# Kernel optimization log

Measured on AMD Instinct MI355X. Metric: run time of the kernel, lower is better.

The kernel has to match this reference:

```python
import jax, jax.numpy as jnp
import numpy as np

B, N, D, H, L, K, V = 2, 2048, 512, 8, 4, 32, 256
HD = D // H
MOD = 4294967296.0
SCALE = 1.0 / np.sqrt(HD)


def _ln(x, g, b):
    m = x.mean(-1, keepdims=True)
    v = ((x - m) ** 2).mean(-1, keepdims=True)
    return (x - m) * jax.lax.rsqrt(v + 1e-5) * g + b


def _expmap0(v, c):
    sc = jnp.sqrt(c)
    vn = jnp.maximum(jnp.linalg.norm(v, axis=-1, keepdims=True), 1e-8)
    return jnp.tanh(sc * vn) * v / (sc * vn)


def _knn_poincare(pos, c):
    xx = jnp.sum(pos ** 2, -1)                                    # [N]
    d2 = jnp.maximum(xx[:, None] + xx[None, :] - 2.0 * pos @ pos.T, 0.0)
    denom = (1.0 - c * xx)[:, None] * (1.0 - c * xx)[None, :] + 1e-8
    arg = jnp.maximum(1.0 + 2.0 * c * d2 / denom, 1.0)
    dist = jnp.arccosh(arg) / jnp.sqrt(c)                         # [N,N]
    neg_d, idx = jax.lax.top_k(-dist, K)                          # smallest-k
    return -neg_d, idx                                            # [N,K],[N,K]


def _forward(hashes, indices, emb, hash_proj, Wb, bb, log_c, pos_tangent,
             Wq, bq, Wk, bk, Wv, bv, Wo, bo, W1, b1, W2, b2,
             g1, be1, g2, be2, log_tau, Wout, bout):
    c = jnp.exp(log_c)
    char = emb[indices]                                           # [B,N,D]
    he = (hashes[..., None].astype(jnp.float32) / MOD) @ hash_proj  # [B,N,D]
    x = jnp.concatenate([char, he], -1) @ Wb + bb                 # [B,N,D]

    # kNN structure computed under no_grad in the original
    pos = _expmap0(jax.lax.stop_gradient(pos_tangent), jax.lax.stop_gradient(c))
    attn_dists, idx = _knn_poincare(pos, jax.lax.stop_gradient(c))  # shared over batch

    for i in range(L):
        xn = _ln(x, g1[i], be1[i])
        q = (xn @ Wq[i] + bq[i]).reshape(B, N, H, HD).transpose(0, 2, 1, 3)
        k = (xn @ Wk[i] + bk[i]).reshape(B, N, H, HD).transpose(0, 2, 1, 3)
        v = (xn @ Wv[i] + bv[i]).reshape(B, N, H, HD).transpose(0, 2, 1, 3)
        kg = k[:, :, idx, :]                                      # [B,H,N,K,HD]
        vg = v[:, :, idx, :]
        fs = jnp.einsum('bhnd,bhnkd->bhnk', q, kg) * SCALE
        gs = -attn_dists[None, None] / (jnp.exp(log_tau[i]) + 1e-8)
        p = jax.nn.softmax(fs + gs, axis=-1)                      # [B,H,N,K]
        ao = jnp.einsum('bhnk,bhnkd->bhnd', p, vg)
        ao = ao.transpose(0, 2, 1, 3).reshape(B, N, D)
        x = x + ao @ Wo[i] + bo[i]
        xn2 = _ln(x, g2[i], be2[i])
        x = x + jax.nn.gelu(xn2 @ W1[i] + b1[i], approximate=False) @ W2[i] + b2[i]

    return x[:, -1, :] @ Wout + bout                              # [B,V]


def setup_inputs():
    key = jax.random.key(0)
    ks = jax.random.split(key, 20)
    rn = lambda k, s, sc=0.02: jax.random.normal(k, s, jnp.float32) * sc
    z = lambda s: jnp.zeros(s, jnp.float32)
    o = lambda s: jnp.ones(s, jnp.float32)
    return {
        'hashes': jax.random.randint(ks[0], (B, N), 0, 1000000),
        'indices': jax.random.randint(ks[1], (B, N), 0, V),
        'emb': rn(ks[2], (V, D)),
        'hash_proj': rn(ks[3], (1, D)),
        'Wb': rn(ks[4], (2 * D, D)),
        'bb': z((D,)),
        'log_c': jnp.array(0.0, jnp.float32),
        'pos_tangent': rn(ks[5], (N, D)),
        'Wq': rn(ks[6], (L, D, D)), 'bq': z((L, D)),
        'Wk': rn(ks[7], (L, D, D)), 'bk': z((L, D)),
        'Wv': rn(ks[8], (L, D, D)), 'bv': z((L, D)),
        'Wo': rn(ks[9], (L, D, D)), 'bo': z((L, D)),
        'W1': rn(ks[10], (L, D, 4 * D)), 'b1': z((L, 4 * D)),
        'W2': rn(ks[11], (L, 4 * D, D)), 'b2': z((L, D)),
        'g1': o((L, D)), 'be1': z((L, D)),
        'g2': o((L, D)), 'be2': z((L, D)),
        'log_tau': z((L,)),
        'Wout': rn(ks[12], (D, V)), 'bout': z((V,)),
    }


def reference(hashes, indices, emb, hash_proj, Wb, bb, log_c, pos_tangent,
              Wq, bq, Wk, bk, Wv, bv, Wo, bo, W1, b1, W2, b2,
              g1, be1, g2, be2, log_tau, Wout, bout):
    return _forward(hashes, indices, emb, hash_proj, Wb, bb, log_c, pos_tangent,
                    Wq, bq, Wk, bk, Wv, bv, Wo, bo, W1, b1, W2, b2,
                    g1, be1, g2, be2, log_tau, Wout, bout)
```

## Files before the change

### kernel.cpp

```cpp
#include <hip/hip_runtime.h>
#include <hip/hip_bf16.h>
#include <math.h>

#define Bb 2
#define Nn 2048
#define Dd 512
#define Hh 8
#define Ll 4
#define Kk 32
#define Vv 256
#define HDh 64
#define Mrows (Bb*Nn)

static constexpr float SCALE_QK = 0.125f;
static constexpr float INV_MOD = 1.0f / 4294967296.0f;

typedef _Float16 f16;
typedef _Float16 f16x8 __attribute__((ext_vector_type(8)));
typedef _Float16 f16x4 __attribute__((ext_vector_type(4)));
typedef _Float16 f16x2 __attribute__((ext_vector_type(2)));
typedef float f32x4 __attribute__((ext_vector_type(4)));

__global__ void scal_kernel(const float* __restrict__ log_c,
                            const float* __restrict__ log_tau,
                            float* __restrict__ scal) {
    int t = threadIdx.x;
    if (t == 0) {
        float c = expf(log_c[0]);
        scal[0] = c;
        scal[1] = sqrtf(c);
    }
    if (t < Ll) scal[2 + t] = 1.0f / (expf(log_tau[t]) + 1e-8f);
}

__global__ __launch_bounds__(256)
void hvec_part_kernel(const float* __restrict__ hash_proj,
                      const float* __restrict__ Wb,
                      float* __restrict__ part) {
    const int b = blockIdx.x;
    const int t = threadIdx.x;
    float a0 = 0.f, a1 = 0.f;
#pragma unroll
    for (int i = 0; i < 16; i++) {
        int kx = b * 16 + i;
        float hp = hash_proj[kx];
        const float* wr = Wb + (size_t)(Dd + kx) * Dd;
        a0 = fmaf(hp, wr[t], a0);
        a1 = fmaf(hp, wr[t + 256], a1);
    }
    part[b * Dd + t]       = a0;
    part[b * Dd + t + 256] = a1;
}
__global__ __launch_bounds__(256)
void hvec_red_kernel(const float* __restrict__ part, float* __restrict__ hvec) {
    const int n = blockIdx.x * 256 + threadIdx.x;
    float acc = 0.f;
#pragma unroll
    for (int b = 0; b < 32; b++) acc += part[b * Dd + n];
    hvec[n] = acc;
}

__global__ void conv_kernel(const float* __restrict__ src, f16* __restrict__ dst, int n) {
    int i = blockIdx.x * 256 + threadIdx.x;
    if (i < n) dst[i] = (f16)src[i];
}

__global__ void pack_bias_kernel(const float* __restrict__ bq, const float* __restrict__ bk,
                                 const float* __restrict__ bv, float* __restrict__ bqkv) {
    int t = blockIdx.x * 256 + threadIdx.x;
    int l = t / 1536, r = t % 1536;
    const float* src = (r < 512) ? bq : ((r < 1024) ? bk : bv);
    bqkv[t] = src[l * 512 + (r & 511)];
}

__global__ __launch_bounds__(256)
void trans_kernel(const float* __restrict__ src, f16* __restrict__ dst,
                  int K, int N, long sStride, long dStride) {
    __shared__ float tile[32][33];
    const float* s = src + blockIdx.z * sStride;
    f16* d = dst + blockIdx.z * dStride;
    int k0 = blockIdx.y * 32, n0 = blockIdx.x * 32;
    int tx = threadIdx.x & 31, ty = threadIdx.x >> 5;
#pragma unroll
    for (int i = 0; i < 32; i += 8)
        tile[ty + i][tx] = s[(long)(k0 + ty + i) * N + n0 + tx];
    __syncthreads();
#pragma unroll
    for (int i = 0; i < 32; i += 8)
        d[(long)(n0 + ty + i) * K + k0 + tx] = (f16)tile[tx][ty + i];
}

__global__ __launch_bounds__(256)
void trans4_kernel(const float* __restrict__ Wq, const float* __restrict__ Wk,
                   const float* __restrict__ Wv, const float* __restrict__ Wo,
                   f16* __restrict__ Wqkvt, f16* __restrict__ Wot) {
    __shared__ float tile[32][33];
    const int which = blockIdx.z >> 2, l = blockIdx.z & 3;
    const float* s;
    f16* d;
    switch (which) {
        case 0: s = Wq + (size_t)l * 262144; d = Wqkvt + (size_t)l * 786432;          break;
        case 1: s = Wk + (size_t)l * 262144; d = Wqkvt + (size_t)l * 786432 + 262144; break;
        case 2: s = Wv + (size_t)l * 262144; d = Wqkvt + (size_t)l * 786432 + 524288; break;
        default:s = Wo + (size_t)l * 262144; d = Wot   + (size_t)l * 262144;          break;
    }
    int k0 = blockIdx.y * 32, n0 = blockIdx.x * 32;
    int tx = threadIdx.x & 31, ty = threadIdx.x >> 5;
#pragma unroll
    for (int i = 0; i < 32; i += 8)
        tile[ty + i][tx] = s[(long)(k0 + ty + i) * 512 + n0 + tx];
    __syncthreads();
#pragma unroll
    for (int i = 0; i < 32; i += 8)
        d[(long)(n0 + ty + i) * 512 + k0 + tx] = (f16)tile[tx][ty + i];
}

template<int TN, bool GATHER, bool RANK1, bool GELU, bool RES, bool OUT16>
__global__ __launch_bounds__(256)
void mgemm(const f16* __restrict__ A, const f16* __restrict__ Wt,
           const float* __restrict__ bias,
           const int* __restrict__ gidx,
           const int* __restrict__ hashes, const float* __restrict__ hvec,
           const float* __restrict__ resid,
           void* __restrict__ Cout, int M, int N, int K) {
    constexpr int TM  = 64;
    constexpr int WRN = (TN == 64) ? 2 : 1;
    constexpr int WCN = 4 / WRN;
    constexpr int WRE = TM / WRN;
    constexpr int NIT = WRE / 16;
    constexpr int ACH = TM * 8;
    constexpr int BCH = TN * 8;
    constexpr int NCH = ACH + BCH;
    constexpr int NCHT = NCH / 256;
    __shared__ __align__(16) f16 sm[NCH * 8];
    const int t = threadIdx.x;
    const int lane = t & 63;
    const int w = t >> 6;
    const int wr = w / WCN, wc = w % WCN;
    const int i0 = blockIdx.y * TM, j0 = blockIdx.x * TN;

    const f16* gsrc[NCHT];
#pragma unroll
    for (int q = 0; q < NCHT; q++) {
        int c = t + q * 256;
        if (c < ACH) {
            int m = c >> 3, kb = (c & 7) ^ (m & 7);
            long row = GATHER ? (long)gidx[i0 + m] : (long)(i0 + m);
            gsrc[q] = A + row * K + kb * 8;
        } else {
            int cc = c - ACH;
            int n = cc >> 3, kb = (cc & 7) ^ (n & 7);
            gsrc[q] = Wt + (long)(j0 + n) * K + kb * 8;
        }
    }

    f32x4 acc[NIT][2];
#pragma unroll
    for (int i = 0; i < NIT; i++)
#pragma unroll
        for (int j = 0; j < 2; j++) acc[i][j] = (f32x4){0.f, 0.f, 0.f, 0.f};

    for (int kt = 0; kt < K; kt += 64) {
        f16x8 stg[NCHT];
#pragma unroll
        for (int q = 0; q < NCHT; q++) stg[q] = *(const f16x8*)(gsrc[q] + kt);
        __syncthreads();
#pragma unroll
        for (int q = 0; q < NCHT; q++)
            *(f16x8*)(sm + (t + q * 256) * 8) = stg[q];
        __syncthreads();

#pragma unroll
        for (int kh = 0; kh < 2; kh++) {
            f16x8 af[NIT], bf[2];
#pragma unroll
            for (int i = 0; i < NIT; i++) {
                int m = wr * WRE + i * 16 + (lane & 15);
                int sl = m * 8 + ((kh * 4 + (lane >> 4)) ^ (m & 7));
                af[i] = *(const f16x8*)(sm + sl * 8);
            }
#pragma unroll
            for (int j = 0; j < 2; j++) {
                int n = wc * 32 + j * 16 + (lane & 15);
                int sl = ACH + n * 8 + ((kh * 4 + (lane >> 4)) ^ (n & 7));
                bf[j] = *(const f16x8*)(sm + sl * 8);
            }
#pragma unroll
            for (int i = 0; i < NIT; i++)
#pragma unroll
                for (int j = 0; j < 2; j++)
                    acc[i][j] = __builtin_amdgcn_mfma_f32_16x16x32_f16(af[i], bf[j], acc[i][j], 0, 0, 0);
        }
    }

    float* Cf = (float*)Cout;
    f16*   Ch = (f16*)Cout;
#pragma unroll
    for (int i = 0; i < NIT; i++) {
        int rbase = i0 + wr * WRE + i * 16 + ((lane >> 4) << 2);
#pragma unroll
        for (int v = 0; v < 4; v++) {
            int row = rbase + v;
            float hterm = RANK1 ? (float)hashes[row] * INV_MOD : 0.f;
#pragma unroll
            for (int j = 0; j < 2; j++) {
                int col = j0 + wc * 32 + j * 16 + (lane & 15);
                float val = acc[i][j][v] + bias[col];
                if (RANK1) val += hterm * hvec[col];
                if (GELU)  val = 0.5f * val * (1.f + erff(val * 0.7071067811865475f));
                if (RES)   val += resid[(long)row * N + col];
                if (OUT16) Ch[(long)row * N + col] = (f16)val;
                else       Cf[(long)row * N + col] = val;
            }
        }
    }
}

__global__ __launch_bounds__(256)
void mdist_kernel(const f16* __restrict__ poshl, const float* __restrict__ xx,
                  const float* __restrict__ scal, float* __restrict__ dist) {
    constexpr int TM = 64, TN = 64;
    constexpr int ACH = TM * 8, BCH = TN * 8, NCH = ACH + BCH;
    constexpr int NCHT = NCH / 256;
    constexpr int KK = 1024;
    __shared__ __align__(16) f16 sm[NCH * 8];
    const int t = threadIdx.x;
    const int lane = t & 63;
    const int w = t >> 6;
    const int wr = w >> 1, wc = w & 1;
    const int i0 = blockIdx.y * TM, j0 = blockIdx.x * TN;

    const f16* gsrc[NCHT];
#pragma unroll
    for (int q = 0; q < NCHT; q++) {
        int c = t + q * 256;
        if (c < ACH) {
            int m = c >> 3, kb = (c & 7) ^ (m & 7);
            gsrc[q] = poshl + (long)(i0 + m) * KK + kb * 8;
        } else {
            int cc = c - ACH;
            int n = cc >> 3, kb = (cc & 7) ^ (n & 7);
            gsrc[q] = poshl + (long)(j0 + n) * KK + kb * 8;
        }
    }

    f32x4 acc[2][2];
#pragma unroll
    for (int i = 0; i < 2; i++)
#pragma unroll
        for (int j = 0; j < 2; j++) acc[i][j] = (f32x4){0.f, 0.f, 0.f, 0.f};

    for (int kt = 0; kt < KK; kt += 64) {
        f16x8 stg[NCHT];
#pragma unroll
        for (int q = 0; q < NCHT; q++) stg[q] = *(const f16x8*)(gsrc[q] + kt);
        __syncthreads();
#pragma unroll
        for (int q = 0; q < NCHT; q++)
            *(f16x8*)(sm + (t + q * 256) * 8) = stg[q];
        __syncthreads();

#pragma unroll
        for (int kh = 0; kh < 2; kh++) {
            f16x8 af[2], bf[2];
#pragma unroll
            for (int i = 0; i < 2; i++) {
                int m = wr * 32 + i * 16 + (lane & 15);
                int sl = m * 8 + ((kh * 4 + (lane >> 4)) ^ (m & 7));
                af[i] = *(const f16x8*)(sm + sl * 8);
            }
#pragma unroll
            for (int j = 0; j < 2; j++) {
                int n = wc * 32 + j * 16 + (lane & 15);
                int sl = ACH + n * 8 + ((kh * 4 + (lane >> 4)) ^ (n & 7));
                bf[j] = *(const f16x8*)(sm + sl * 8);
            }
#pragma unroll
            for (int i = 0; i < 2; i++)
#pragma unroll
                for (int j = 0; j < 2; j++)
                    acc[i][j] = __builtin_amdgcn_mfma_f32_16x16x32_f16(af[i], bf[j], acc[i][j], 0, 0, 0);
        }
    }

    const float c = scal[0];
#pragma unroll
    for (int i = 0; i < 2; i++) {
        int rbase = i0 + wr * 32 + i * 16 + ((lane >> 4) << 2);
#pragma unroll
        for (int v = 0; v < 4; v++) {
            int row = rbase + v;
            float xi = xx[row];
#pragma unroll
            for (int j = 0; j < 2; j++) {
                int col = j0 + wc * 32 + j * 16 + (lane & 15);
                float xj = xx[col];
                float d2 = fmaxf(xi + xj - 2.f * acc[i][j][v], 0.f);
                float denom = (1.f - c * xi) * (1.f - c * xj) + 1e-8f;
                float arg = fmaxf(1.f + 2.f * c * d2 / denom, 1.f);
                dist[(long)row * Nn + col] = arg;
            }
        }
    }
}

__global__ __launch_bounds__(64)
void ln_kernel(const float* __restrict__ x, const float* __restrict__ g,
               const float* __restrict__ be, f16* __restrict__ xn) {
    const int row = blockIdx.x, t = threadIdx.x;
    const float4* xr = (const float4*)(x + (size_t)row * Dd);
    float4 v0 = xr[t], v1 = xr[t + 64];
    float s = v0.x + v0.y + v0.z + v0.w + v1.x + v1.y + v1.z + v1.w;
#pragma unroll
    for (int off = 32; off; off >>= 1) s += __shfl_xor(s, off, 64);
    float mean = s * (1.f / Dd);
    float d0x = v0.x - mean, d0y = v0.y - mean, d0z = v0.z - mean, d0w = v0.w - mean;
    float d1x = v1.x - mean, d1y = v1.y - mean, d1z = v1.z - mean, d1w = v1.w - mean;
    float q = d0x*d0x + d0y*d0y + d0z*d0z + d0w*d0w
            + d1x*d1x + d1y*d1y + d1z*d1z + d1w*d1w;
#pragma unroll
    for (int off = 32; off; off >>= 1) q += __shfl_xor(q, off, 64);
    float rstd = rsqrtf(q * (1.f / Dd) + 1e-5f);
    float4 g0 = ((const float4*)g)[t], g1v = ((const float4*)g)[t + 64];
    float4 b0 = ((const float4*)be)[t], b1v = ((const float4*)be)[t + 64];
    f16* xo = xn + (size_t)row * Dd;
    f16x4 o0, o1;
    o0[0] = (f16)(d0x * rstd * g0.x + b0.x);
    o0[1] = (f16)(d0y * rstd * g0.y + b0.y);
    o0[2] = (f16)(d0z * rstd * g0.z + b0.z);
    o0[3] = (f16)(d0w * rstd * g0.w + b0.w);
    o1[0] = (f16)(d1x * rstd * g1v.x + b1v.x);
    o1[1] = (f16)(d1y * rstd * g1v.y + b1v.y);
    o1[2] = (f16)(d1z * rstd * g1v.z + b1v.z);
    o1[3] = (f16)(d1w * rstd * g1v.w + b1v.w);
    *(f16x4*)(xo + t * 4)         = o0;
    *(f16x4*)(xo + (t + 64) * 4)  = o1;
}

__global__ __launch_bounds__(256)
void expmap_kernel(const float* __restrict__ vt, const float* __restrict__ scal,
                   f16* __restrict__ poshl, float* __restrict__ xx) {
    __shared__ float red[256];
    const int row = blockIdx.x, t = threadIdx.x;
    const float* vr = vt + (size_t)row * Dd;
    float v0 = vr[t], v1 = vr[t + 256];
    red[t] = v0 * v0 + v1 * v1;
    __syncthreads();
    for (int off = 128; off; off >>= 1) {
        if (t < off) red[t] += red[t + off];
        __syncthreads();
    }
    float total = red[0];
    float vn = fmaxf(sqrtf(total), 1e-8f);
    float sc = scal[1];
    float factor = tanhf(sc * vn) / (sc * vn);
    float p0 = factor * v0, p1 = factor * v1;
    f16 h0 = (f16)p0, h1 = (f16)p1;
    f16* pr = poshl + (size_t)row * 1024;
    pr[t]             = h0;
    pr[t + 256]       = h1;
    pr[512 + t]       = (f16)(p0 - (float)h0);
    pr[512 + t + 256] = (f16)(p1 - (float)h1);
    if (t == 0) xx[row] = factor * factor * total;
}

__global__ __launch_bounds__(64)
void topk_kernel(const float* __restrict__ dist, const float* __restrict__ scal,
                 float* __restrict__ outd, int* __restrict__ outi) {
    const int lane = threadIdx.x;
    const int n = blockIdx.x;
    const float sqc = scal[1];
    const float* dr = dist + (size_t)n * Nn;
    float val[32];
#pragma unroll
    for (int i = 0; i < 32; i++) val[i] = dr[i * 64 + lane];
    float lmin = val[0];
    int   li   = 0;
#pragma unroll
    for (int i = 1; i < 32; i++) {
        if (val[i] < lmin) { lmin = val[i]; li = i; }
    }

    for (int s = 0; s < Kk; s++) {
        float wmin = lmin;
#pragma unroll
        for (int off = 32; off; off >>= 1)
            wmin = fminf(wmin, __shfl_xor(wmin, off, 64));
        const bool tiedl = (lmin == wmin);
        unsigned long long tied = __ballot(tiedl);
        const int gidx = li * 64 + lane;
        bool owner;
        if (__popcll(tied) == 1) {
            owner = tiedl;
        } else {
            int cand = tiedl ? gidx : 0x7FFFFFFF;
#pragma unroll
            for (int off = 32; off; off >>= 1)
                cand = min(cand, __shfl_xor(cand, off, 64));
            owner = tiedl && (gidx == cand);
        }
        if (owner) {
            outd[n * Kk + s] = acoshf(wmin) / sqc;
            outi[n * Kk + s] = gidx;
#pragma unroll
            for (int i = 0; i < 32; i++)
                if (i == li) val[i] = 3.0e38f;
            lmin = val[0]; li = 0;
#pragma unroll
            for (int i = 1; i < 32; i++) {
                if (val[i] < lmin) { lmin = val[i]; li = i; }
            }
        }
    }
}

#define KVSTR 520
__global__ __launch_bounds__(256)
void attn_kernel(const f16* __restrict__ qkv, const float* __restrict__ adist,
                 const int* __restrict__ aidx, const float* __restrict__ scal,
                 int layer, f16* __restrict__ ao) {
    __shared__ __align__(16) f16 kv[64 * KVSTR];
    __shared__ __align__(16) f16 qs[512];
    __shared__ float ps[Hh][Kk];
    __shared__ float sdist[Kk];
    __shared__ int   sidx[Kk];
    const int t = threadIdx.x;
    const int b = blockIdx.x >> 11, n = blockIdx.x & (Nn - 1);
    const float inv_tau = scal[2 + layer];

    if (t < Kk) {
        sidx[t]  = aidx[n * Kk + t];
        sdist[t] = adist[n * Kk + t];
    }
    __syncthreads();

    {
        const size_t qrow = (size_t)(b * Nn + n) * 1536;
#pragma unroll
        for (int q = 0; q < 16; q++) {
            int c = q * 256 + t;
            int j = c >> 7, ci = c & 127;
            size_t src = (size_t)(b * Nn + sidx[j]) * 1536 + 512 + ci * 8;
            int dst = (ci < 64) ? (j * KVSTR + ci * 8)
                                : ((32 + j) * KVSTR + (ci - 64) * 8);
            *(f16x8*)(kv + dst) = *(const f16x8*)(qkv + src);
        }
        if (t < 64) *(f16x8*)(qs + t * 8) = *(const f16x8*)(qkv + qrow + t * 8);
    }
    __syncthreads();

    const int h = t >> 5, j = t & 31;
    float dot = 0.f;
#pragma unroll
    for (int i = 0; i < 8; i++) {
        f16x8 qa = *(const f16x8*)(qs + h * HDh + i * 8);
        f16x8 ka = *(const f16x8*)(kv + j * KVSTR + h * HDh + i * 8);
#pragma unroll
        for (int m = 0; m < 4; m++) {
            f16x2 qp = {qa[2 * m], qa[2 * m + 1]};
            f16x2 kp = {ka[2 * m], ka[2 * m + 1]};
            dot = __builtin_amdgcn_fdot2(qp, kp, dot, false);
        }
    }
    float s = dot * SCALE_QK - sdist[j] * inv_tau;
    float mx = s;
#pragma unroll
    for (int off = 16; off; off >>= 1) mx = fmaxf(mx, __shfl_xor(mx, off, 64));
    float e = expf(s - mx);
    float sum = e;
#pragma unroll
    for (int off = 16; off; off >>= 1) sum += __shfl_xor(sum, off, 64);
    ps[h][j] = e / sum;
    __syncthreads();

    const int d2 = t & 31;
    float a0 = 0.f, a1 = 0.f;
#pragma unroll
    for (int jj = 0; jj < Kk; jj++) {
        float p = ps[h][jj];
        f16x2 vv = *(const f16x2*)(kv + (32 + jj) * KVSTR + h * HDh + d2 * 2);
        a0 = fmaf(p, (float)vv[0], a0);
        a1 = fmaf(p, (float)vv[1], a1);
    }
    f16x2 outv; outv[0] = (f16)a0; outv[1] = (f16)a1;
    *(f16x2*)(ao + (size_t)(b * Nn + n) * Dd + h * HDh + d2 * 2) = outv;
}

__global__ void out_kernel(const float* __restrict__ x, const float* __restrict__ Wout,
                           const float* __restrict__ bout, float* __restrict__ out) {
    const int b = blockIdx.x, vc = threadIdx.x;
    const float* xr = x + ((size_t)(b * Nn + (Nn - 1))) * Dd;
    float acc = bout[vc];
    for (int d = 0; d < Dd; d++) acc = fmaf(xr[d], Wout[(size_t)d * Vv + vc], acc);
    out[b * Vv + vc] = acc;
}

static constexpr size_t X_OFF     = 0;
static constexpr size_t XN16_OFF  = 8388608;
static constexpr size_t QKV16_OFF = 12582912;
static constexpr size_t AO16_OFF  = 25165824;
static constexpr size_t H1_OFF    = 29360128;
static constexpr size_t AD_OFF    = 46137344;
static constexpr size_t AI_OFF    = 46399488;
static constexpr size_t SC_OFF    = 46661632;
static constexpr size_t HV_OFF    = 46661888;
static constexpr size_t XX_OFF    = 46663936;
static constexpr size_t BQKV_OFF  = 46672128;
static constexpr size_t EMB16_OFF = 46704896;
static constexpr size_t WBT_OFF   = 46967040;
static constexpr size_t WQKVT_OFF = 47491328;
static constexpr size_t WOT_OFF   = 53782784;
static constexpr size_t W1T_OFF   = 55879936;
static constexpr size_t W2T_OFF   = 64268544;
static constexpr size_t HP_OFF    = 72657152;

extern "C" void kernel_launch(void* const* d_in, const int* in_sizes, int n_in,
                              void* d_out, int out_size, void* d_ws, size_t ws_size,
                              hipStream_t stream) {
    (void)in_sizes; (void)n_in; (void)out_size; (void)ws_size;
    const int*   hashes    = (const int*)  d_in[0];
    const int*   indices   = (const int*)  d_in[1];
    const float* emb       = (const float*)d_in[2];
    const float* hash_proj = (const float*)d_in[3];
    const float* Wb        = (const float*)d_in[4];
    const float* bb        = (const float*)d_in[5];
    const float* log_c     = (const float*)d_in[6];
    const float* pos_t     = (const float*)d_in[7];
    const float* Wq        = (const float*)d_in[8];
    const float* bq        = (const float*)d_in[9];
    const float* Wk        = (const float*)d_in[10];
    const float* bk        = (const float*)d_in[11];
    const float* Wv        = (const float*)d_in[12];
    const float* bv        = (const float*)d_in[13];
    const float* Wo        = (const float*)d_in[14];
    const float* bo        = (const float*)d_in[15];
    const float* W1        = (const float*)d_in[16];
    const float* b1        = (const float*)d_in[17];
    const float* W2        = (const float*)d_in[18];
    const float* b2        = (const float*)d_in[19];
    const float* g1        = (const float*)d_in[20];
    const float* be1       = (const float*)d_in[21];
    const float* g2        = (const float*)d_in[22];
    const float* be2       = (const float*)d_in[23];
    const float* log_tau   = (const float*)d_in[24];
    const float* Wout      = (const float*)d_in[25];
    const float* bout      = (const float*)d_in[26];

    char* ws = (char*)d_ws;
    float* x      = (float*)(ws + X_OFF);
    f16*   xn16   = (f16*)  (ws + XN16_OFF);
    f16*   qkv16  = (f16*)  (ws + QKV16_OFF);
    f16*   ao16   = (f16*)  (ws + AO16_OFF);
    f16*   h1     = (f16*)  (ws + H1_OFF);
    float* adist  = (float*)(ws + AD_OFF);
    int*   aidx   = (int*)  (ws + AI_OFF);
    float* scal   = (float*)(ws + SC_OFF);
    float* hvec   = (float*)(ws + HV_OFF);
    float* xxb    = (float*)(ws + XX_OFF);
    float* bqkv   = (float*)(ws + BQKV_OFF);
    f16*   emb16  = (f16*)  (ws + EMB16_OFF);
    f16*   Wbt    = (f16*)  (ws + WBT_OFF);
    f16*   Wqkvt  = (f16*)  (ws + WQKVT_OFF);
    f16*   Wot    = (f16*)  (ws + WOT_OFF);
    f16*   W1t    = (f16*)  (ws + W1T_OFF);
    f16*   W2t    = (f16*)  (ws + W2T_OFF);
    float* hpart  = (float*)(ws + HP_OFF);
    f16*   poshl  = (f16*)  (ws + AO16_OFF);
    float* distb  = (float*)(ws + H1_OFF);

    scal_kernel<<<1, 64, 0, stream>>>(log_c, log_tau, scal);
    hvec_part_kernel<<<32, 256, 0, stream>>>(hash_proj, Wb, hpart);
    hvec_red_kernel<<<2, 256, 0, stream>>>(hpart, hvec);
    pack_bias_kernel<<<24, 256, 0, stream>>>(bq, bk, bv, bqkv);
    conv_kernel<<<(Vv * Dd + 255) / 256, 256, 0, stream>>>(emb, emb16, Vv * Dd);
    trans_kernel<<<dim3(16, 16, 1), 256, 0, stream>>>(Wb, Wbt, 512, 512, 0, 0);
    trans4_kernel<<<dim3(16, 16, 16), 256, 0, stream>>>(Wq, Wk, Wv, Wo, Wqkvt, Wot);
    trans_kernel<<<dim3(64, 16, Ll), 256, 0, stream>>>(W1, W1t, 512, 2048, 1048576, 1048576);
    trans_kernel<<<dim3(16, 64, Ll), 256, 0, stream>>>(W2, W2t, 2048, 512, 1048576, 1048576);

    mgemm<64, true, true, false, false, false><<<dim3(8, 64), 256, 0, stream>>>(
        emb16, Wbt, bb, indices, hashes, hvec, nullptr, x, Mrows, Dd, Dd);

    expmap_kernel<<<Nn, 256, 0, stream>>>(pos_t, scal, poshl, xxb);
    mdist_kernel<<<dim3(32, 32), 256, 0, stream>>>(poshl, xxb, scal, distb);
    topk_kernel<<<Nn, 64, 0, stream>>>(distb, scal, adist, aidx);

    for (int l = 0; l < Ll; l++) {
        ln_kernel<<<Mrows, 64, 0, stream>>>(x, g1 + l * Dd, be1 + l * Dd, xn16);
        mgemm<128, false, false, false, false, true><<<dim3(12, 64), 256, 0, stream>>>(
            xn16, Wqkvt + (size_t)l * 786432, bqkv + l * 1536,
            nullptr, nullptr, nullptr, nullptr, qkv16, Mrows, 1536, Dd);
        attn_kernel<<<Bb * Nn, 256, 0, stream>>>(qkv16, adist, aidx, scal, l, ao16);
        mgemm<64, false, false, false, true, false><<<dim3(8, 64), 256, 0, stream>>>(
            ao16, Wot + (size_t)l * 262144, bo + l * Dd,
            nullptr, nullptr, nullptr, x, x, Mrows, Dd, Dd);
        ln_kernel<<<Mrows, 64, 0, stream>>>(x, g2 + l * Dd, be2 + l * Dd, xn16);
        mgemm<128, false, false, true, false, true><<<dim3(16, 64), 256, 0, stream>>>(
            xn16, W1t + (size_t)l * 1048576, b1 + l * 4 * Dd,
            nullptr, nullptr, nullptr, nullptr, h1, Mrows, 4 * Dd, Dd);
        mgemm<64, false, false, false, true, false><<<dim3(8, 64), 256, 0, stream>>>(
            h1, W2t + (size_t)l * 1048576, b2 + l * Dd,
            nullptr, nullptr, nullptr, x, x, Mrows, Dd, 4 * Dd);
    }

    out_kernel<<<Bb, Vv, 0, stream>>>(x, Wout, bout, (float*)d_out);
}
```

Before: 670.0 us.

## Replace iterative top-k selection with register bitonic sort and cross-lane merge

The top-k kernel used to run 32 serial rounds of a wave-wide argmin with ballots and rescans. It now packs each distance bit pattern with its column index into a 64-bit key and bitonic-sorts 32 keys per lane in registers. It then runs six butterfly merge levels across lanes, each keeping the 32 smallest keys, so lane i ends up holding the i-th nearest neighbor. Ties break by lowest index through the key ordering. In exchange it does many more compare-swaps and 64-bit shuffles, with higher register pressure.

```diff
diff --git a/kernel.cpp b/kernel.cpp
--- a/kernel.cpp
+++ b/kernel.cpp
@@ -20,6 +20,7 @@
 typedef _Float16 f16x4 __attribute__((ext_vector_type(4)));
 typedef _Float16 f16x2 __attribute__((ext_vector_type(2)));
 typedef float f32x4 __attribute__((ext_vector_type(4)));
+typedef unsigned long long u64;
 
 __global__ void scal_kernel(const float* __restrict__ log_c,
                             const float* __restrict__ log_tau,
@@ -364,53 +365,82 @@
     if (t == 0) xx[row] = factor * factor * total;
 }
 
+__device__ __forceinline__ u64 shfl_xor_u64(u64 v, int d) {
+    int lo = __shfl_xor((int)(unsigned)v, d, 64);
+    int hi = __shfl_xor((int)(unsigned)(v >> 32), d, 64);
+    return ((u64)(unsigned)hi << 32) | (u64)(unsigned)lo;
+}
+
 __global__ __launch_bounds__(64)
 void topk_kernel(const float* __restrict__ dist, const float* __restrict__ scal,
                  float* __restrict__ outd, int* __restrict__ outi) {
     const int lane = threadIdx.x;
     const int n = blockIdx.x;
     const float sqc = scal[1];
-    const float* dr = dist + (size_t)n * Nn;
-    float val[32];
-#pragma unroll
-    for (int i = 0; i < 32; i++) val[i] = dr[i * 64 + lane];
-    float lmin = val[0];
-    int   li   = 0;
-#pragma unroll
-    for (int i = 1; i < 32; i++) {
-        if (val[i] < lmin) { lmin = val[i]; li = i; }
-    }
-
-    for (int s = 0; s < Kk; s++) {
-        float wmin = lmin;
-#pragma unroll
-        for (int off = 32; off; off >>= 1)
-            wmin = fminf(wmin, __shfl_xor(wmin, off, 64));
-        const bool tiedl = (lmin == wmin);
-        unsigned long long tied = __ballot(tiedl);
-        const int gidx = li * 64 + lane;
-        bool owner;
-        if (__popcll(tied) == 1) {
-            owner = tiedl;
-        } else {
-            int cand = tiedl ? gidx : 0x7FFFFFFF;
-#pragma unroll
-            for (int off = 32; off; off >>= 1)
-                cand = min(cand, __shfl_xor(cand, off, 64));
-            owner = tiedl && (gidx == cand);
-        }
-        if (owner) {
-            outd[n * Kk + s] = acoshf(wmin) / sqc;
-            outi[n * Kk + s] = gidx;
-#pragma unroll
-            for (int i = 0; i < 32; i++)
-                if (i == li) val[i] = 3.0e38f;
-            lmin = val[0]; li = 0;
-#pragma unroll
-            for (int i = 1; i < 32; i++) {
-                if (val[i] < lmin) { lmin = val[i]; li = i; }
-            }
-        }
+    const float4* dr4 = (const float4*)(dist + (size_t)n * Nn);
+
+    u64 key[32];
+#pragma unroll
+    for (int q = 0; q < 8; q++) {
+        float4 v = dr4[lane + q * 64];
+        int g = (lane + q * 64) * 4;
+        key[q * 4 + 0] = ((u64)__float_as_uint(v.x) << 11) | (u64)(g + 0);
+        key[q * 4 + 1] = ((u64)__float_as_uint(v.y) << 11) | (u64)(g + 1);
+        key[q * 4 + 2] = ((u64)__float_as_uint(v.z) << 11) | (u64)(g + 2);
+        key[q * 4 + 3] = ((u64)__float_as_uint(v.w) << 11) | (u64)(g + 3);
+    }
+
+#pragma unroll
+    for (int k = 2; k <= 32; k <<= 1) {
+#pragma unroll
+        for (int j = k >> 1; j > 0; j >>= 1) {
+#pragma unroll
+            for (int i = 0; i < 32; i++) {
+                int l = i ^ j;
+                if (l > i) {
+                    bool up = ((i & k) == 0);
+                    u64 a = key[i], b = key[l];
+                    bool sw = up ? (a > b) : (a < b);
+                    key[i] = sw ? b : a;
+                    key[l] = sw ? a : b;
+                }
+            }
+        }
+    }
+
+#pragma unroll
+    for (int dlev = 0; dlev < 6; dlev++) {
+        const int d = 1 << dlev;
+#pragma unroll
+        for (int t = 0; t < 16; t++) {
+            const int u = 31 - t;
+            u64 bt = shfl_xor_u64(key[u], d);
+            u64 bu = shfl_xor_u64(key[t], d);
+            key[t] = (key[t] < bt) ? key[t] : bt;
+            key[u] = (key[u] < bu) ? key[u] : bu;
+        }
+#pragma unroll
+        for (int j = 16; j > 0; j >>= 1) {
+#pragma unroll
+            for (int i = 0; i < 32; i++) {
+                if ((i & j) == 0) {
+                    const int l = i | j;
+                    u64 a = key[i], b = key[l];
+                    bool sw = (a > b);
+                    key[i] = sw ? b : a;
+                    key[l] = sw ? a : b;
+                }
+            }
+        }
+    }
+
+    u64 mykey = key[0];
+#pragma unroll
+    for (int i = 1; i < 32; i++) mykey = (lane == i) ? key[i] : mykey;
+    if (lane < Kk) {
+        float v = __uint_as_float((unsigned)(mykey >> 11));
+        outd[n * Kk + lane] = acoshf(v) / sqc;
+        outi[n * Kk + lane] = (int)(mykey & 2047u);
     }
 }
 
```

New measurement: 681.1 us. Within noise of the previous version (+1.6%).

## Replace iterative top-k selection with radix bisection threshold plus rank sort

Applied to the files above, without the earlier changes.

The top-k kernel now uses 256 threads per row and binary-searches on the float bit pattern to find a threshold that admits between 32 and 96 candidates. The survivors are compacted into shared memory with atomics and ranked by pairwise comparison of packed (value, index) keys, with a tie-handling fallback. This replaces 32 serial wave-wide min reductions per row with a roughly logarithmic number of count passes. It adds block-level syncs per bisection step, and the top-k kernel is a small part of the total runtime.

```diff
diff --git a/kernel.cpp b/kernel.cpp
--- a/kernel.cpp
+++ b/kernel.cpp
@@ -20,6 +20,7 @@
 typedef _Float16 f16x4 __attribute__((ext_vector_type(4)));
 typedef _Float16 f16x2 __attribute__((ext_vector_type(2)));
 typedef float f32x4 __attribute__((ext_vector_type(4)));
+typedef unsigned long long u64;
 
 __global__ void scal_kernel(const float* __restrict__ log_c,
                             const float* __restrict__ log_tau,
@@ -364,51 +365,110 @@
     if (t == 0) xx[row] = factor * factor * total;
 }
 
-__global__ __launch_bounds__(64)
+__global__ __launch_bounds__(256)
 void topk_kernel(const float* __restrict__ dist, const float* __restrict__ scal,
                  float* __restrict__ outd, int* __restrict__ outi) {
-    const int lane = threadIdx.x;
+    __shared__ unsigned wred[4];
+    __shared__ unsigned bc;
+    __shared__ __align__(8) u64 buf[128];
+    const int t = threadIdx.x;
+    const int w = t >> 6;
     const int n = blockIdx.x;
     const float sqc = scal[1];
-    const float* dr = dist + (size_t)n * Nn;
-    float val[32];
-#pragma unroll
-    for (int i = 0; i < 32; i++) val[i] = dr[i * 64 + lane];
-    float lmin = val[0];
-    int   li   = 0;
-#pragma unroll
-    for (int i = 1; i < 32; i++) {
-        if (val[i] < lmin) { lmin = val[i]; li = i; }
-    }
-
-    for (int s = 0; s < Kk; s++) {
-        float wmin = lmin;
-#pragma unroll
-        for (int off = 32; off; off >>= 1)
-            wmin = fminf(wmin, __shfl_xor(wmin, off, 64));
-        const bool tiedl = (lmin == wmin);
-        unsigned long long tied = __ballot(tiedl);
-        const int gidx = li * 64 + lane;
-        bool owner;
-        if (__popcll(tied) == 1) {
-            owner = tiedl;
-        } else {
-            int cand = tiedl ? gidx : 0x7FFFFFFF;
-#pragma unroll
-            for (int off = 32; off; off >>= 1)
-                cand = min(cand, __shfl_xor(cand, off, 64));
-            owner = tiedl && (gidx == cand);
-        }
-        if (owner) {
-            outd[n * Kk + s] = acoshf(wmin) / sqc;
-            outi[n * Kk + s] = gidx;
-#pragma unroll
-            for (int i = 0; i < 32; i++)
-                if (i == li) val[i] = 3.0e38f;
-            lmin = val[0]; li = 0;
-#pragma unroll
-            for (int i = 1; i < 32; i++) {
-                if (val[i] < lmin) { lmin = val[i]; li = i; }
+    const uint4* dr = (const uint4*)(dist + (size_t)n * Nn);
+
+    uint4 va = dr[t * 2];
+    uint4 vb = dr[t * 2 + 1];
+    unsigned k[8] = {va.x, va.y, va.z, va.w, vb.x, vb.y, vb.z, vb.w};
+    const int g0 = t * 8;
+
+    unsigned lo = 0x3F800000u;
+    unsigned hi = 0x7F800001u;
+    unsigned chi = 2048u;
+    while (chi > 96u && (hi - lo) > 1u) {
+        unsigned mid = lo + ((hi - lo) >> 1);
+        int c = 0;
+#pragma unroll
+        for (int j = 0; j < 8; j++) c += (k[j] < mid) ? 1 : 0;
+#pragma unroll
+        for (int off = 32; off; off >>= 1) c += __shfl_xor(c, off, 64);
+        __syncthreads();
+        if ((t & 63) == 0) wred[w] = (unsigned)c;
+        __syncthreads();
+        unsigned ct = wred[0] + wred[1] + wred[2] + wred[3];
+        if (ct >= 32u) { hi = mid; chi = ct; } else { lo = mid; }
+    }
+
+    if (chi <= 96u) {
+        if (t == 0) bc = 0u;
+        __syncthreads();
+#pragma unroll
+        for (int j = 0; j < 8; j++) {
+            if (k[j] < hi) {
+                unsigned s = atomicAdd(&bc, 1u);
+                buf[s] = ((u64)k[j] << 11) | (u64)(unsigned)(g0 + j);
+            }
+        }
+        __syncthreads();
+        const int m = (int)chi;
+        if (t < m) {
+            u64 my = buf[t];
+            int r = 0;
+            for (int j = 0; j < m; j++) r += (buf[j] < my) ? 1 : 0;
+            if (r < Kk) {
+                float v = __uint_as_float((unsigned)(my >> 11));
+                outd[n * Kk + r] = acoshf(v) / sqc;
+                outi[n * Kk + r] = (int)(my & 2047u);
+            }
+        }
+    } else {
+        int c = 0;
+#pragma unroll
+        for (int j = 0; j < 8; j++) c += (k[j] < lo) ? 1 : 0;
+#pragma unroll
+        for (int off = 32; off; off >>= 1) c += __shfl_xor(c, off, 64);
+        __syncthreads();
+        if ((t & 63) == 0) wred[w] = (unsigned)c;
+        if (t == 0) bc = 0u;
+        __syncthreads();
+        const int cless = (int)(wred[0] + wred[1] + wred[2] + wred[3]);
+#pragma unroll
+        for (int j = 0; j < 8; j++) {
+            if (k[j] < lo) {
+                unsigned s = atomicAdd(&bc, 1u);
+                buf[s] = ((u64)k[j] << 11) | (u64)(unsigned)(g0 + j);
+            }
+        }
+        __syncthreads();
+        if (t < cless) {
+            u64 my = buf[t];
+            int r = 0;
+            for (int j = 0; j < cless; j++) r += (buf[j] < my) ? 1 : 0;
+            float v = __uint_as_float((unsigned)(my >> 11));
+            outd[n * Kk + r] = acoshf(v) / sqc;
+            outi[n * Kk + r] = (int)(my & 2047u);
+        }
+        const int need = Kk - cless;
+        unsigned eqm = 0u;
+#pragma unroll
+        for (int j = 0; j < 8; j++) if (k[j] == lo) eqm |= (1u << j);
+        const float dv = acoshf(__uint_as_float(lo)) / sqc;
+        for (int s = 0; s < need; s++) {
+            int mi = 0x7FFFFFFF;
+#pragma unroll
+            for (int j = 0; j < 8; j++)
+                if (eqm & (1u << j)) mi = min(mi, g0 + j);
+#pragma unroll
+            for (int off = 32; off; off >>= 1) mi = min(mi, __shfl_xor(mi, off, 64));
+            __syncthreads();
+            if ((t & 63) == 0) wred[w] = (unsigned)mi;
+            __syncthreads();
+            int m4 = (int)min(min(wred[0], wred[1]), min(wred[2], wred[3]));
+            int j = m4 - g0;
+            if (j >= 0 && j < 8 && (eqm & (1u << j))) {
+                eqm &= ~(1u << j);
+                outd[n * Kk + cless + s] = dv;
+                outi[n * Kk + cless + s] = m4;
             }
         }
     }
@@ -583,7 +643,7 @@
 
     expmap_kernel<<<Nn, 256, 0, stream>>>(pos_t, scal, poshl, xxb);
     mdist_kernel<<<dim3(32, 32), 256, 0, stream>>>(poshl, xxb, scal, distb);
-    topk_kernel<<<Nn, 64, 0, stream>>>(distb, scal, adist, aidx);
+    topk_kernel<<<Nn, 256, 0, stream>>>(distb, scal, adist, aidx);
 
     for (int l = 0; l < Ll; l++) {
         ln_kernel<<<Mrows, 64, 0, stream>>>(x, g1 + l * Dd, be1 + l * Dd, xn16);
```

Result: faster. 639.2 us (-4.6%).
